# Optimization experiments

Hardware: AMD Instinct MI355X
Metric: run time of the kernel (lower is better)

## Reference

```python
import jax, jax.numpy as jnp
import numpy as np

B = 64        # batch
V1 = 4096     # nodes, layer 1 (D)
V2 = 1024     # nodes after pool/4
DF = 8        # input features (DFeat)
K1 = 25       # Chebyshev order layer 1
K2 = 25       # Chebyshev order layer 2
F1 = 32       # CL1_F
F2 = 64       # CL2_F
FC1F = 512    # FC1_F
FC2F = 10     # FC2_F
E1 = 65536    # nnz of L1
E2 = 16384    # nnz of L2
FC1Fin = F2 * (V1 // 16)  # 16384


def setup_inputs() -> dict:
    key = jax.random.key(0)
    ks = jax.random.split(key, 16)
    x = jax.random.normal(ks[0], (B, V1, DF), jnp.float32)
    L1_rows = jax.random.randint(ks[1], (E1,), 0, V1, dtype=jnp.int32)
    L1_cols = jax.random.randint(ks[2], (E1,), 0, V1, dtype=jnp.int32)
    # small values keep the order-25 Chebyshev recursion numerically tame
    L1_vals = jax.random.normal(ks[3], (E1,), jnp.float32) * 0.05
    L2_rows = jax.random.randint(ks[4], (E2,), 0, V2, dtype=jnp.int32)
    L2_cols = jax.random.randint(ks[5], (E2,), 0, V2, dtype=jnp.int32)
    L2_vals = jax.random.normal(ks[6], (E2,), jnp.float32) * 0.05

    def glorot(k, shape, fin, fout):
        s = np.sqrt(2.0 / (fin + fout)).astype(np.float32)
        return jax.random.uniform(k, shape, jnp.float32, -s, s)

    cl1_w = glorot(ks[7], (F1, K1 * DF), K1, F1)
    cl1_b = jnp.zeros((F1,), jnp.float32)
    cl2_w = glorot(ks[8], (F2, K2 * F1), K2 * F1, F2)
    cl2_b = jnp.zeros((F2,), jnp.float32)
    fc1_w = glorot(ks[9], (FC1F, FC1Fin), FC1Fin, FC1F)
    fc1_b = jnp.zeros((FC1F,), jnp.float32)
    fc2_w = glorot(ks[10], (FC2F, FC1F), FC1F, FC2F)
    fc2_b = jnp.zeros((FC2F,), jnp.float32)
    return dict(x=x, L1_rows=L1_rows, L1_cols=L1_cols, L1_vals=L1_vals,
                L2_rows=L2_rows, L2_cols=L2_cols, L2_vals=L2_vals,
                cl1_w=cl1_w, cl1_b=cl1_b, cl2_w=cl2_w, cl2_b=cl2_b,
                fc1_w=fc1_w, fc1_b=fc1_b, fc2_w=fc2_w, fc2_b=fc2_b)


def _cheb_conv(x, rows, cols, vals, W, b, K):
    """Chebyshev graph conv. x: [B, V, Fin]; sparse L as COO edge lists."""
    Bb, V, Fin = x.shape
    x0 = x.transpose(1, 2, 0).reshape(V, Fin * Bb)  # [V, Fin*B]

    def spmm(y):  # sparse [V,V] @ dense [V, C]
        return jax.ops.segment_sum(vals[:, None] * y[cols], rows, num_segments=V)

    x1 = spmm(x0)

    def step(carry, _):
        xm2, xm1 = carry
        xk = 2.0 * spmm(xm1) - xm2
        return (xm1, xk), xk

    _, rest = jax.lax.scan(step, (x0, x1), None, length=K - 2)
    stack = jnp.concatenate([x0[None], x1[None], rest], axis=0)  # [K, V, Fin*B]
    # [K,V,Fin,B] -> [B,V,Fin,K] -> [B*V, Fin*K], matching torch layout
    feat = stack.reshape(K, V, Fin, Bb).transpose(3, 1, 2, 0).reshape(Bb * V, Fin * K)
    out = feat @ W.T + b
    return out.reshape(Bb, V, -1)


def _max_pool(x, p):
    Bb, V, F = x.shape
    return x.reshape(Bb, V // p, p, F).max(axis=2)


def reference(x, L1_rows, L1_cols, L1_vals, L2_rows, L2_cols, L2_vals,
              cl1_w, cl1_b, cl2_w, cl2_b, fc1_w, fc1_b, fc2_w, fc2_b):
    h = _cheb_conv(x, L1_rows, L1_cols, L1_vals, cl1_w, cl1_b, K1)
    h = jax.nn.relu(h)
    h = _max_pool(h, 4)                                   # [B, V/4, F1]
    h = _cheb_conv(h, L2_rows, L2_cols, L2_vals, cl2_w, cl2_b, K2)
    h = jax.nn.relu(h)
    h = _max_pool(h, 4)                                   # [B, V/16, F2]
    h = h.reshape(-1, FC1Fin)
    h = jax.nn.relu(h @ fc1_w.T + fc1_b)
    # dropout treated as identity (eval mode / d=0)
    return h @ fc2_w.T + fc2_b                            # [B, FC2F]
```

## Files before the change

kernel.cpp:

```cpp
#include <hip/hip_runtime.h>
#include <hip/hip_fp16.h>

#define B_    64
#define V1_   4096
#define V2_   1024
#define DF_   8
#define K_    25
#define NP_   13
#define F1_   32
#define F2_   64
#define FC1F_ 512
#define FC2F_ 10
#define E1_   65536
#define E2_   16384
#define C1_   512
#define C2_   2048
#define FCIN_ 16384

typedef short bf16x8 __attribute__((ext_vector_type(8)));
typedef float f32x4  __attribute__((ext_vector_type(4)));

#define FMA_MIX_LO(acc, qv, gv) \
    asm("v_fma_mix_f32 %0, %1, %2, %0 op_sel:[1,0,0] op_sel_hi:[1,1,0]" \
        : "+v"(acc) : "v"(qv), "v"(gv))
#define FMA_MIX_HI(acc, qv, gv) \
    asm("v_fma_mix_f32 %0, %1, %2, %0 op_sel:[1,1,0] op_sel_hi:[1,1,0]" \
        : "+v"(acc) : "v"(qv), "v"(gv))

__device__ __forceinline__ unsigned short f2bf(float x) {
    unsigned u = __float_as_uint(x);
    u += 0x7FFFu + ((u >> 16) & 1u);
    return (unsigned short)(u >> 16);
}
__device__ __forceinline__ float h2f_lo(unsigned u) {
    return __half2float(__ushort_as_half((unsigned short)(u & 0xFFFFu)));
}
__device__ __forceinline__ float h2f_hi(unsigned u) {
    return __half2float(__ushort_as_half((unsigned short)(u >> 16)));
}

__global__ __launch_bounds__(256) void k_transpose_x(const float* __restrict__ x,
                                                     float* __restrict__ X0T) {
    __shared__ float tsh[DF_][B_][16];
    const int t = threadIdx.x;
    const int v0 = blockIdx.x * 16;
    for (int rep = 0; rep < 4; ++rep) {
        int idx = rep*256 + t;
        int b = idx >> 4, vv = idx & 15;
        const float4* p = (const float4*)&x[((size_t)b*V1_ + v0 + vv)*DF_];
        float4 a0 = p[0], a1 = p[1];
        tsh[0][b][vv]=a0.x; tsh[1][b][vv]=a0.y; tsh[2][b][vv]=a0.z; tsh[3][b][vv]=a0.w;
        tsh[4][b][vv]=a1.x; tsh[5][b][vv]=a1.y; tsh[6][b][vv]=a1.z; tsh[7][b][vv]=a1.w;
    }
    __syncthreads();
    for (int rep = 0; rep < 32; ++rep) {
        int idx = rep*256 + t;
        int vv = idx & 15, b = (idx >> 4) & 63, fin = idx >> 10;
        X0T[(size_t)(fin*64 + b)*V1_ + v0 + vv] = tsh[fin][b][vv];
    }
}

__global__ __launch_bounds__(256) void k_count(const int* __restrict__ rows, int E,
                                               int* __restrict__ cnt) {
    int e = blockIdx.x*256 + threadIdx.x;
    if (e < E) atomicAdd(&cnt[rows[e]], 1);
}

__global__ __launch_bounds__(256) void k_scan(const int* __restrict__ cnt, int V,
                                              int* __restrict__ offs, int* __restrict__ cursor) {
    __shared__ int psum[256];
    int t = threadIdx.x;
    int chunk = V >> 8;
    int lo = t*chunk;
    int s = 0;
    for (int i = lo; i < lo+chunk; ++i) s += (cnt[i] + 3) & ~3;
    psum[t] = s;
    __syncthreads();
    for (int off = 1; off < 256; off <<= 1) {
        int val = (t >= off) ? psum[t-off] : 0;
        __syncthreads();
        psum[t] += val;
        __syncthreads();
    }
    int run = (t == 0) ? 0 : psum[t-1];
    for (int i = lo; i < lo+chunk; ++i) {
        offs[i] = run; cursor[i] = run;
        run += (cnt[i] + 3) & ~3;
    }
    if (t == 255) offs[V] = run;
}

__global__ __launch_bounds__(256) void k_scatter(const int* __restrict__ rows,
                                                 const int* __restrict__ cols,
                                                 const float* __restrict__ vals, int E,
                                                 int shift,
                                                 int* __restrict__ cursor,
                                                 unsigned* __restrict__ ep) {
    int e = blockIdx.x*256 + threadIdx.x;
    if (e < E) {
        int p = atomicAdd(&cursor[rows[e]], 1);
        unsigned hv = (unsigned)__half_as_ushort(__float2half(vals[e]));
        ep[p] = (hv << 16) | ((unsigned)cols[e] << shift);
    }
}

template<int V, int THREADS, int MINW>
__global__ __launch_bounds__(THREADS, MINW) void k_cheb1(
        const float* __restrict__ X0T,
        const int* __restrict__ offs,
        const unsigned* __restrict__ ep,
        unsigned* __restrict__ stk) {
    constexpr int RPT = V / THREADS;
    __shared__ unsigned buf[2*V];
    const int c0 = blockIdx.x*2;
    const int t = threadIdx.x;
    int e0r[RPT], e1r[RPT];
    unsigned tlo0[RPT], tlo1[RPT];
    unsigned* __restrict__ p0 = stk + (size_t)(c0+0)*NP_*V;
    unsigned* __restrict__ p1 = stk + (size_t)(c0+1)*NP_*V;

#pragma unroll
    for (int r = 0; r < RPT; ++r) {
        const int v = r*THREADS + t;
        e0r[r] = offs[v]; e1r[r] = offs[v+1];
        const float x0 = X0T[(size_t)c0*V + v];
        const float x1 = X0T[(size_t)(c0+1)*V + v];
        __half2 hh = __floats2half2_rn(x0, x1);
        buf[v] = *(const unsigned*)&hh;
        tlo0[r] = f2bf(x0); tlo1[r] = f2bf(x1);
    }
    __syncthreads();

    auto step = [&](const unsigned* __restrict__ src, unsigned* __restrict__ dst,
                    bool first, bool last, int plane) {
#pragma unroll
        for (int r = 0; r < RPT; ++r) {
            const int v = r*THREADS + t;
            float s0a=0.f,s0b=0.f,s0c=0.f,s0d=0.f;
            float s1a=0.f,s1b=0.f,s1c=0.f,s1d=0.f;
            const int ee0 = e0r[r], ee1 = e1r[r];
            uint4 q = *(const uint4*)&ep[ee0];
            for (int e = ee0; e < ee1; e += 4) {
                const uint4 qn = *(const uint4*)&ep[e + 4];
                const unsigned g0 = *(const unsigned*)((const char*)src + (q.x & 0xFFFFu));
                const unsigned g1 = *(const unsigned*)((const char*)src + (q.y & 0xFFFFu));
                const unsigned g2 = *(const unsigned*)((const char*)src + (q.z & 0xFFFFu));
                const unsigned g3 = *(const unsigned*)((const char*)src + (q.w & 0xFFFFu));
                FMA_MIX_LO(s0a, q.x, g0); FMA_MIX_HI(s1a, q.x, g0);
                FMA_MIX_LO(s0b, q.y, g1); FMA_MIX_HI(s1b, q.y, g1);
                FMA_MIX_LO(s0c, q.z, g2); FMA_MIX_HI(s1c, q.z, g2);
                FMA_MIX_LO(s0d, q.w, g3); FMA_MIX_HI(s1d, q.w, g3);
                q = qn;
            }
            const float g0s = (s0a+s0b)+(s0c+s0d);
            const float g1s = (s1a+s1b)+(s1c+s1d);
            float xn0, xn1;
            if (first) { xn0 = g0s; xn1 = g1s; }
            else {
                const unsigned old = dst[v];
                xn0 = fmaf(2.f, g0s, -h2f_lo(old));
                xn1 = fmaf(2.f, g1s, -h2f_hi(old));
            }
            if (!last) {
                __half2 hh = __floats2half2_rn(xn0, xn1);
                dst[v] = *(const unsigned*)&hh;
            }
            const unsigned h0 = f2bf(xn0), h1 = f2bf(xn1);
            if (plane < 0) { tlo0[r] = h0; tlo1[r] = h1; }
            else {
                p0[(size_t)plane*V + v] = tlo0[r] | (h0 << 16);
                p1[(size_t)plane*V + v] = tlo1[r] | (h1 << 16);
            }
        }
        __syncthreads();
    };

    step(buf, buf + V, true, false, 0);
    for (int k = 2; k < 24; k += 2) {
        step(buf + V, buf, false, false, -1);
        step(buf, buf + V, false, false, (k + 1) >> 1);
    }
    step(buf + V, buf, false, true, -1);

#pragma unroll
    for (int r = 0; r < RPT; ++r) {
        const int v = r*THREADS + t;
        p0[(size_t)12*V + v] = tlo0[r];
        p1[(size_t)12*V + v] = tlo1[r];
    }
}

template<int V, int THREADS, int MINW>
__global__ __launch_bounds__(THREADS, MINW) void k_cheb2(
        const float* __restrict__ X0T,
        const int* __restrict__ offs,
        const unsigned* __restrict__ ep,
        unsigned* __restrict__ stk) {
    constexpr int RPT = V / THREADS;
    __shared__ uint2 buf[2*V];
    const int c0 = blockIdx.x*4;
    const int t = threadIdx.x;
    int e0r[RPT], e1r[RPT];
    unsigned tlo[RPT][4];
    unsigned* __restrict__ pl[4];
#pragma unroll
    for (int j = 0; j < 4; ++j) pl[j] = stk + (size_t)(c0+j)*NP_*V;

#pragma unroll
    for (int r = 0; r < RPT; ++r) {
        const int v = r*THREADS + t;
        e0r[r] = offs[v]; e1r[r] = offs[v+1];
        float xj[4];
#pragma unroll
        for (int j = 0; j < 4; ++j) {
            xj[j] = X0T[(size_t)(c0+j)*V + v];
            tlo[r][j] = f2bf(xj[j]);
        }
        __half2 ha = __floats2half2_rn(xj[0], xj[1]);
        __half2 hb = __floats2half2_rn(xj[2], xj[3]);
        buf[v] = make_uint2(*(const unsigned*)&ha, *(const unsigned*)&hb);
    }
    __syncthreads();

    auto step = [&](const uint2* __restrict__ src, uint2* __restrict__ dst,
                    bool first, bool last, int plane) {
#pragma unroll
        for (int r = 0; r < RPT; ++r) {
            const int v = r*THREADS + t;
            float acc[4][4];
#pragma unroll
            for (int j = 0; j < 4; ++j)
#pragma unroll
                for (int i = 0; i < 4; ++i) acc[j][i] = 0.f;
            const int ee0 = e0r[r], ee1 = e1r[r];
            uint4 q = *(const uint4*)&ep[ee0];
            for (int e = ee0; e < ee1; e += 4) {
                const uint4 qn = *(const uint4*)&ep[e + 4];
                const uint2 g0 = *(const uint2*)((const char*)src + (q.x & 0xFFFFu));
                const uint2 g1 = *(const uint2*)((const char*)src + (q.y & 0xFFFFu));
                const uint2 g2 = *(const uint2*)((const char*)src + (q.z & 0xFFFFu));
                const uint2 g3 = *(const uint2*)((const char*)src + (q.w & 0xFFFFu));
                FMA_MIX_LO(acc[0][0], q.x, g0.x); FMA_MIX_HI(acc[1][0], q.x, g0.x);
                FMA_MIX_LO(acc[2][0], q.x, g0.y); FMA_MIX_HI(acc[3][0], q.x, g0.y);
                FMA_MIX_LO(acc[0][1], q.y, g1.x); FMA_MIX_HI(acc[1][1], q.y, g1.x);
                FMA_MIX_LO(acc[2][1], q.y, g1.y); FMA_MIX_HI(acc[3][1], q.y, g1.y);
                FMA_MIX_LO(acc[0][2], q.z, g2.x); FMA_MIX_HI(acc[1][2], q.z, g2.x);
                FMA_MIX_LO(acc[2][2], q.z, g2.y); FMA_MIX_HI(acc[3][2], q.z, g2.y);
                FMA_MIX_LO(acc[0][3], q.w, g3.x); FMA_MIX_HI(acc[1][3], q.w, g3.x);
                FMA_MIX_LO(acc[2][3], q.w, g3.y); FMA_MIX_HI(acc[3][3], q.w, g3.y);
                q = qn;
            }
            float gs[4];
#pragma unroll
            for (int j = 0; j < 4; ++j)
                gs[j] = (acc[j][0]+acc[j][1])+(acc[j][2]+acc[j][3]);
            float xn[4];
            if (first) {
#pragma unroll
                for (int j = 0; j < 4; ++j) xn[j] = gs[j];
            } else {
                const uint2 old = dst[v];
                xn[0] = fmaf(2.f, gs[0], -h2f_lo(old.x));
                xn[1] = fmaf(2.f, gs[1], -h2f_hi(old.x));
                xn[2] = fmaf(2.f, gs[2], -h2f_lo(old.y));
                xn[3] = fmaf(2.f, gs[3], -h2f_hi(old.y));
            }
            if (!last) {
                __half2 ha = __floats2half2_rn(xn[0], xn[1]);
                __half2 hb = __floats2half2_rn(xn[2], xn[3]);
                dst[v] = make_uint2(*(const unsigned*)&ha, *(const unsigned*)&hb);
            }
            unsigned h[4];
#pragma unroll
            for (int j = 0; j < 4; ++j) h[j] = f2bf(xn[j]);
            if (plane < 0) {
#pragma unroll
                for (int j = 0; j < 4; ++j) tlo[r][j] = h[j];
            } else {
#pragma unroll
                for (int j = 0; j < 4; ++j)
                    pl[j][(size_t)plane*V + v] = tlo[r][j] | (h[j] << 16);
            }
        }
        __syncthreads();
    };

    step(buf, buf + V, true, false, 0);
    for (int k = 2; k < 24; k += 2) {
        step(buf + V, buf, false, false, -1);
        step(buf, buf + V, false, false, (k + 1) >> 1);
    }
    step(buf + V, buf, false, true, -1);

#pragma unroll
    for (int r = 0; r < RPT; ++r) {
        const int v = r*THREADS + t;
#pragma unroll
        for (int j = 0; j < 4; ++j)
            pl[j][(size_t)12*V + v] = tlo[r][j];
    }
}

template<int FIN, int F>
__global__ __launch_bounds__(256) void k_wprep(const float* __restrict__ W,
                                               unsigned short* __restrict__ Wb) {
    int idx = blockIdx.x*256 + threadIdx.x;
    int kk  = idx & 7;
    int f   = (idx >> 3) % F;
    int g   = (idx >> 3) / F % 4;
    int fin = idx / (8*F*4);
    int k = g*8 + kk;
    Wb[idx] = (k < K_) ? f2bf(W[(size_t)f*(FIN*K_) + fin*K_ + k]) : 0;
}

__global__ __launch_bounds__(256) void k_gemm1(const unsigned* __restrict__ STK,
                                               const unsigned short* __restrict__ Wb,
                                               const float* __restrict__ bias,
                                               float* __restrict__ X0T2) {
    __shared__ float Tsm[32][36];
    const int t = threadIdx.x, lane = t & 63, wave = t >> 6;
    const int b = blockIdx.x;
    const int v0 = blockIdx.y*128 + wave*32;
    const int m = lane & 15, g = lane >> 4;
    int offp[4];
#pragma unroll
    for (int p = 0; p < 4; ++p) {
        int pl = 4*g + p; if (pl > 12) pl = 12;
        offp[p] = pl*V1_ + v0 + m;
    }

    f32x4 acc[2][2];
#pragma unroll
    for (int mt = 0; mt < 2; ++mt)
#pragma unroll
        for (int ft = 0; ft < 2; ++ft) acc[mt][ft] = (f32x4){0.f,0.f,0.f,0.f};

#pragma unroll
    for (int fin = 0; fin < DF_; ++fin) {
        const unsigned* sp = STK + (size_t)(fin*64 + b)*(NP_*V1_);
        unsigned ua[4], ub[4];
#pragma unroll
        for (int p = 0; p < 4; ++p) { ua[p] = sp[offp[p]]; ub[p] = sp[offp[p] + 16]; }
        bf16x8 a0, a1;
        __builtin_memcpy(&a0, ua, 16);
        __builtin_memcpy(&a1, ub, 16);
        const bf16x8 w0 = *(const bf16x8*)&Wb[((fin*4+g)*F1_ + m)*8];
        const bf16x8 w1 = *(const bf16x8*)&Wb[((fin*4+g)*F1_ + 16 + m)*8];
        acc[0][0] = __builtin_amdgcn_mfma_f32_16x16x32_bf16(a0, w0, acc[0][0], 0,0,0);
        acc[0][1] = __builtin_amdgcn_mfma_f32_16x16x32_bf16(a0, w1, acc[0][1], 0,0,0);
        acc[1][0] = __builtin_amdgcn_mfma_f32_16x16x32_bf16(a1, w0, acc[1][0], 0,0,0);
        acc[1][1] = __builtin_amdgcn_mfma_f32_16x16x32_bf16(a1, w1, acc[1][1], 0,0,0);
    }
    float bv[2] = { bias[m], bias[16+m] };
#pragma unroll
    for (int mt = 0; mt < 2; ++mt)
#pragma unroll
        for (int ft = 0; ft < 2; ++ft) {
            f32x4 a = acc[mt][ft];
            float mx = fmaxf(fmaxf(a[0],a[1]), fmaxf(a[2],a[3])) + bv[ft];
            Tsm[ft*16 + m][wave*8 + mt*4 + g] = fmaxf(mx, 0.f);
        }
    __syncthreads();
    const int f = t >> 3, vg = t & 7;
    float4 o = *(const float4*)&Tsm[f][vg*4];
    *(float4*)&X0T2[(size_t)(f*64+b)*V2_ + blockIdx.y*32 + vg*4] = o;
}

__global__ __launch_bounds__(256) void k_gemm2(const unsigned* __restrict__ STK,
                                               const unsigned short* __restrict__ Wb,
                                               const float* __restrict__ bias,
                                               float* __restrict__ FCINT) {
    const int t = threadIdx.x, lane = t & 63, wave = t >> 6;
    const int b = blockIdx.x;
    const int v0 = blockIdx.y*128 + wave*32;
    const int m = lane & 15, g = lane >> 4;
    int offp[4];
#pragma unroll
    for (int p = 0; p < 4; ++p) {
        int pl = 4*g + p; if (pl > 12) pl = 12;
        offp[p] = pl*V2_ + v0 + m;
    }

    f32x4 acc[2][4];
#pragma unroll
    for (int mt = 0; mt < 2; ++mt)
#pragma unroll
        for (int ft = 0; ft < 4; ++ft) acc[mt][ft] = (f32x4){0.f,0.f,0.f,0.f};

#pragma unroll 4
    for (int fin = 0; fin < F1_; ++fin) {
        const unsigned* sp = STK + (size_t)(fin*64 + b)*(NP_*V2_);
        unsigned ua[4], ub[4];
#pragma unroll
        for (int p = 0; p < 4; ++p) { ua[p] = sp[offp[p]]; ub[p] = sp[offp[p] + 16]; }
        bf16x8 a0, a1;
        __builtin_memcpy(&a0, ua, 16);
        __builtin_memcpy(&a1, ub, 16);
#pragma unroll
        for (int ft = 0; ft < 4; ++ft) {
            const bf16x8 bw = *(const bf16x8*)&Wb[((fin*4+g)*F2_ + ft*16 + m)*8];
            acc[0][ft] = __builtin_amdgcn_mfma_f32_16x16x32_bf16(a0, bw, acc[0][ft], 0,0,0);
            acc[1][ft] = __builtin_amdgcn_mfma_f32_16x16x32_bf16(a1, bw, acc[1][ft], 0,0,0);
        }
    }
#pragma unroll
    for (int mt = 0; mt < 2; ++mt)
#pragma unroll
        for (int ft = 0; ft < 4; ++ft) {
            f32x4 a = acc[mt][ft];
            float mx = fmaxf(fmaxf(a[0],a[1]), fmaxf(a[2],a[3])) + bias[ft*16 + m];
            mx = fmaxf(mx, 0.f);
            int v2 = blockIdx.y*32 + wave*8 + mt*4 + g;
            FCINT[((size_t)v2*64 + ft*16 + m)*64 + b] = mx;
        }
}

__global__ __launch_bounds__(256) void k_fc1_init(const float* __restrict__ bias,
                                                  float* __restrict__ O) {
    int idx = blockIdx.x*256 + threadIdx.x;
    O[idx] = bias[idx & (FC1F_-1)];
}

__global__ __launch_bounds__(256) void k_fc1(const float* __restrict__ AT,
                                             const float* __restrict__ W,
                                             float* __restrict__ O) {
    const int t = threadIdx.x;
    const int b = t & 63;
    const int jq = __builtin_amdgcn_readfirstlane(t >> 6);
    const int j0 = blockIdx.x*32 + jq*8;
    const int i0 = blockIdx.y*1024;
    float acc[8] = {};
    for (int i = i0; i < i0 + 1024; i += 4) {
        float a0 = AT[(size_t)(i+0)*64 + b];
        float a1 = AT[(size_t)(i+1)*64 + b];
        float a2 = AT[(size_t)(i+2)*64 + b];
        float a3 = AT[(size_t)(i+3)*64 + b];
#pragma unroll
        for (int jj = 0; jj < 8; ++jj) {
            const float* wp = &W[(size_t)(j0+jj)*FCIN_ + i];
            acc[jj] = fmaf(a0, wp[0], acc[jj]);
            acc[jj] = fmaf(a1, wp[1], acc[jj]);
            acc[jj] = fmaf(a2, wp[2], acc[jj]);
            acc[jj] = fmaf(a3, wp[3], acc[jj]);
        }
    }
#pragma unroll
    for (int jj = 0; jj < 8; ++jj)
        atomicAdd(&O[b*FC1F_ + j0 + jj], acc[jj]);
}

__global__ void k_fc2(const float* __restrict__ O1, const float* __restrict__ W2,
                      const float* __restrict__ b2, float* __restrict__ out) {
    int c = blockIdx.x;
    int b = threadIdx.x;
    float s = b2[c];
    for (int j = 0; j < FC1F_; ++j)
        s = fmaf(fmaxf(O1[b*FC1F_ + j], 0.f), W2[c*FC1F_ + j], s);
    out[b*FC2F_ + c] = s;
}

extern "C" void kernel_launch(void* const* d_in, const int* in_sizes, int n_in,
                              void* d_out, int out_size, void* d_ws, size_t ws_size,
                              hipStream_t stream) {
    const float* x   = (const float*)d_in[0];
    const int*   l1r = (const int*)d_in[1];
    const int*   l1c = (const int*)d_in[2];
    const float* l1v = (const float*)d_in[3];
    const int*   l2r = (const int*)d_in[4];
    const int*   l2c = (const int*)d_in[5];
    const float* l2v = (const float*)d_in[6];
    const float* w1  = (const float*)d_in[7];
    const float* b1  = (const float*)d_in[8];
    const float* w2  = (const float*)d_in[9];
    const float* b2  = (const float*)d_in[10];
    const float* fw1 = (const float*)d_in[11];
    const float* fb1 = (const float*)d_in[12];
    const float* fw2 = (const float*)d_in[13];
    const float* fb2 = (const float*)d_in[14];
    float* out = (float*)d_out;

    char* wsp = (char*)d_ws;
    size_t off = 0;
    auto alloc = [&](size_t bytes) -> void* {
        void* p = wsp + off;
        off += (bytes + 255) & ~size_t(255);
        return p;
    };
    float*    X0T1  = (float*)alloc((size_t)C1_*V1_*4);
    unsigned* STACK = (unsigned*)alloc((size_t)C1_*NP_*V1_*4);
    float*    X0T2  = (float*)alloc((size_t)C2_*V2_*4);
    float*    FCINT = (float*)alloc((size_t)FCIN_*B_*4);
    float*    FC1O  = (float*)alloc((size_t)B_*FC1F_*4);
    unsigned short* WB1 = (unsigned short*)alloc((size_t)DF_*4*F1_*8*2);
    unsigned short* WB2 = (unsigned short*)alloc((size_t)F1_*4*F2_*8*2);
    int*      cnt1  = (int*)alloc(V1_*4);
    int*      offs1 = (int*)alloc((V1_+1)*4);
    int*      cur1  = (int*)alloc(V1_*4);
    unsigned* ep1   = (unsigned*)alloc((size_t)(E1_ + 4*V1_ + 8)*4);
    int*      cnt2  = (int*)alloc(V2_*4);
    int*      offs2 = (int*)alloc((V2_+1)*4);
    int*      cur2  = (int*)alloc(V2_*4);
    unsigned* ep2   = (unsigned*)alloc((size_t)(E2_ + 4*V2_ + 8)*4);

    hipMemsetAsync(cnt1, 0, V1_*4, stream);
    hipMemsetAsync(ep1, 0, (size_t)(E1_ + 4*V1_ + 8)*4, stream);
    hipMemsetAsync(cnt2, 0, V2_*4, stream);
    hipMemsetAsync(ep2, 0, (size_t)(E2_ + 4*V2_ + 8)*4, stream);
    hipLaunchKernelGGL(k_count,   dim3(E1_/256), dim3(256), 0, stream, l1r, E1_, cnt1);
    hipLaunchKernelGGL(k_scan,    dim3(1),       dim3(256), 0, stream, cnt1, V1_, offs1, cur1);
    hipLaunchKernelGGL(k_scatter, dim3(E1_/256), dim3(256), 0, stream, l1r, l1c, l1v, E1_, 2, cur1, ep1);
    hipLaunchKernelGGL(k_count,   dim3(E2_/256), dim3(256), 0, stream, l2r, E2_, cnt2);
    hipLaunchKernelGGL(k_scan,    dim3(1),       dim3(256), 0, stream, cnt2, V2_, offs2, cur2);
    hipLaunchKernelGGL(k_scatter, dim3(E2_/256), dim3(256), 0, stream, l2r, l2c, l2v, E2_, 3, cur2, ep2);
    hipLaunchKernelGGL((k_wprep<DF_,F1_>), dim3(DF_*4*F1_*8/256), dim3(256), 0, stream, w1, WB1);
    hipLaunchKernelGGL((k_wprep<F1_,F2_>), dim3(F1_*4*F2_*8/256), dim3(256), 0, stream, w2, WB2);

    hipLaunchKernelGGL(k_transpose_x, dim3(V1_/16), dim3(256), 0, stream, x, X0T1);
    hipLaunchKernelGGL((k_cheb1<V1_,1024,4>), dim3(C1_/2), dim3(1024), 0, stream,
                       X0T1, offs1, ep1, STACK);
    hipLaunchKernelGGL(k_gemm1, dim3(64, 32), dim3(256), 0, stream, STACK, WB1, b1, X0T2);

    hipLaunchKernelGGL((k_cheb2<V2_,512,4>), dim3(C2_/4), dim3(512), 0, stream,
                       X0T2, offs2, ep2, STACK);
    hipLaunchKernelGGL(k_gemm2, dim3(64, 8), dim3(256), 0, stream, STACK, WB2, b2, FCINT);

    hipLaunchKernelGGL(k_fc1_init, dim3(B_*FC1F_/256), dim3(256), 0, stream, fb1, FC1O);
    hipLaunchKernelGGL(k_fc1, dim3(16, 16), dim3(256), 0, stream, FCINT, fw1, FC1O);
    hipLaunchKernelGGL(k_fc2, dim3(FC2F_), dim3(B_), 0, stream, FC1O, fw2, fb2, out);
}
```

Before: 640.6 us.

## Split layer-1 Chebyshev rows across block pairs with global flag exchange

The layer-1 Chebyshev kernel now processes four channels per block, packed as two half2 values in shared memory, so each edge gather serves twice as many columns. Each channel group's node rows are split across two cooperating blocks. After every recursion step the two blocks trade their half of the new vector through a global exchange buffer, synchronised with release/acquire flag spin-waits. The intent is to keep the same 256-block grid with a 64KB shared buffer while halving per-block edge work. The risks are deadlock if the paired blocks are not co-resident, plus added per-step global traffic and spin latency.

```diff
diff --git a/kernel.cpp b/kernel.cpp
--- a/kernel.cpp
+++ b/kernel.cpp
@@ -16,6 +16,7 @@
 #define C1_   512
 #define C2_   2048
 #define FCIN_ 16384
+#define NPAIR1_ (C1_/4)
 
 typedef short bf16x8 __attribute__((ext_vector_type(8)));
 typedef float f32x4  __attribute__((ext_vector_type(4)));
@@ -104,89 +105,139 @@
     }
 }
 
-template<int V, int THREADS, int MINW>
-__global__ __launch_bounds__(THREADS, MINW) void k_cheb1(
+template<int V, int THREADS>
+__global__ __launch_bounds__(THREADS, 4) void k_cheb1(
         const float* __restrict__ X0T,
         const int* __restrict__ offs,
         const unsigned* __restrict__ ep,
-        unsigned* __restrict__ stk) {
-    constexpr int RPT = V / THREADS;
-    __shared__ unsigned buf[2*V];
-    const int c0 = blockIdx.x*2;
+        unsigned* __restrict__ stk,
+        uint2* __restrict__ xchg,
+        int* __restrict__ flags) {
+    constexpr int HV  = V/2;
+    constexpr int RPT = HV / THREADS;
+    __shared__ uint2 buf[2*V];
+    const int p = blockIdx.x >> 1, h = blockIdx.x & 1;
+    const int c0 = p*4;
+    const int row0 = h*HV;
     const int t = threadIdx.x;
     int e0r[RPT], e1r[RPT];
-    unsigned tlo0[RPT], tlo1[RPT];
-    unsigned* __restrict__ p0 = stk + (size_t)(c0+0)*NP_*V;
-    unsigned* __restrict__ p1 = stk + (size_t)(c0+1)*NP_*V;
-
+    unsigned tlo[RPT][4];
+    unsigned* __restrict__ pl[4];
+#pragma unroll
+    for (int j = 0; j < 4; ++j) pl[j] = stk + (size_t)(c0+j)*NP_*V;
+
+    for (int i = 0; i < V/THREADS; ++i) {
+        const int v = i*THREADS + t;
+        float xj[4];
+#pragma unroll
+        for (int j = 0; j < 4; ++j) xj[j] = X0T[(size_t)(c0+j)*V + v];
+        __half2 ha = __floats2half2_rn(xj[0], xj[1]);
+        __half2 hb = __floats2half2_rn(xj[2], xj[3]);
+        buf[v] = make_uint2(*(const unsigned*)&ha, *(const unsigned*)&hb);
+    }
 #pragma unroll
     for (int r = 0; r < RPT; ++r) {
-        const int v = r*THREADS + t;
+        const int v = row0 + r*THREADS + t;
         e0r[r] = offs[v]; e1r[r] = offs[v+1];
-        const float x0 = X0T[(size_t)c0*V + v];
-        const float x1 = X0T[(size_t)(c0+1)*V + v];
-        __half2 hh = __floats2half2_rn(x0, x1);
-        buf[v] = *(const unsigned*)&hh;
-        tlo0[r] = f2bf(x0); tlo1[r] = f2bf(x1);
+#pragma unroll
+        for (int j = 0; j < 4; ++j) tlo[r][j] = f2bf(X0T[(size_t)(c0+j)*V + v]);
     }
     __syncthreads();
 
-    auto step = [&](const unsigned* __restrict__ src, unsigned* __restrict__ dst,
-                    bool first, bool last, int plane) {
+    for (int k = 1; k <= 24; ++k) {
+        const bool first = (k == 1), last = (k == 24);
+        const int plane = (k & 1) ? (k >> 1) : -1;
+        const uint2* __restrict__ src = buf + ((k & 1) ? 0 : V);
+        uint2*       __restrict__ dst = buf + ((k & 1) ? V : 0);
+        const int xbase = (((k & 1)*NPAIR1_ + p)*2 + h)*HV;
+
 #pragma unroll
         for (int r = 0; r < RPT; ++r) {
-            const int v = r*THREADS + t;
-            float s0a=0.f,s0b=0.f,s0c=0.f,s0d=0.f;
-            float s1a=0.f,s1b=0.f,s1c=0.f,s1d=0.f;
+            const int v = row0 + r*THREADS + t;
+            float acc[4][4];
+#pragma unroll
+            for (int j = 0; j < 4; ++j)
+#pragma unroll
+                for (int i = 0; i < 4; ++i) acc[j][i] = 0.f;
             const int ee0 = e0r[r], ee1 = e1r[r];
             uint4 q = *(const uint4*)&ep[ee0];
             for (int e = ee0; e < ee1; e += 4) {
                 const uint4 qn = *(const uint4*)&ep[e + 4];
-                const unsigned g0 = *(const unsigned*)((const char*)src + (q.x & 0xFFFFu));
-                const unsigned g1 = *(const unsigned*)((const char*)src + (q.y & 0xFFFFu));
-                const unsigned g2 = *(const unsigned*)((const char*)src + (q.z & 0xFFFFu));
-                const unsigned g3 = *(const unsigned*)((const char*)src + (q.w & 0xFFFFu));
-                FMA_MIX_LO(s0a, q.x, g0); FMA_MIX_HI(s1a, q.x, g0);
-                FMA_MIX_LO(s0b, q.y, g1); FMA_MIX_HI(s1b, q.y, g1);
-                FMA_MIX_LO(s0c, q.z, g2); FMA_MIX_HI(s1c, q.z, g2);
-                FMA_MIX_LO(s0d, q.w, g3); FMA_MIX_HI(s1d, q.w, g3);
+                const uint2 g0 = *(const uint2*)((const char*)src + (q.x & 0xFFFFu));
+                const uint2 g1 = *(const uint2*)((const char*)src + (q.y & 0xFFFFu));
+                const uint2 g2 = *(const uint2*)((const char*)src + (q.z & 0xFFFFu));
+                const uint2 g3 = *(const uint2*)((const char*)src + (q.w & 0xFFFFu));
+                FMA_MIX_LO(acc[0][0], q.x, g0.x); FMA_MIX_HI(acc[1][0], q.x, g0.x);
+                FMA_MIX_LO(acc[2][0], q.x, g0.y); FMA_MIX_HI(acc[3][0], q.x, g0.y);
+                FMA_MIX_LO(acc[0][1], q.y, g1.x); FMA_MIX_HI(acc[1][1], q.y, g1.x);
+                FMA_MIX_LO(acc[2][1], q.y, g1.y); FMA_MIX_HI(acc[3][1], q.y, g1.y);
+                FMA_MIX_LO(acc[0][2], q.z, g2.x); FMA_MIX_HI(acc[1][2], q.z, g2.x);
+                FMA_MIX_LO(acc[2][2], q.z, g2.y); FMA_MIX_HI(acc[3][2], q.z, g2.y);
+                FMA_MIX_LO(acc[0][3], q.w, g3.x); FMA_MIX_HI(acc[1][3], q.w, g3.x);
+                FMA_MIX_LO(acc[2][3], q.w, g3.y); FMA_MIX_HI(acc[3][3], q.w, g3.y);
                 q = qn;
             }
-            const float g0s = (s0a+s0b)+(s0c+s0d);
-            const float g1s = (s1a+s1b)+(s1c+s1d);
-            float xn0, xn1;
-            if (first) { xn0 = g0s; xn1 = g1s; }
-            else {
-                const unsigned old = dst[v];
-                xn0 = fmaf(2.f, g0s, -h2f_lo(old));
-                xn1 = fmaf(2.f, g1s, -h2f_hi(old));
-            }
+            float gs[4], xn[4];
+#pragma unroll
+            for (int j = 0; j < 4; ++j)
+                gs[j] = (acc[j][0]+acc[j][1])+(acc[j][2]+acc[j][3]);
+            if (first) {
+#pragma unroll
+                for (int j = 0; j < 4; ++j) xn[j] = gs[j];
+            } else {
+                const uint2 old = dst[v];
+                xn[0] = fmaf(2.f, gs[0], -h2f_lo(old.x));
+                xn[1] = fmaf(2.f, gs[1], -h2f_hi(old.x));
+                xn[2] = fmaf(2.f, gs[2], -h2f_lo(old.y));
+                xn[3] = fmaf(2.f, gs[3], -h2f_hi(old.y));
+            }
+            __half2 ha = __floats2half2_rn(xn[0], xn[1]);
+            __half2 hb = __floats2half2_rn(xn[2], xn[3]);
+            const uint2 pk = make_uint2(*(const unsigned*)&ha, *(const unsigned*)&hb);
             if (!last) {
-                __half2 hh = __floats2half2_rn(xn0, xn1);
-                dst[v] = *(const unsigned*)&hh;
-            }
-            const unsigned h0 = f2bf(xn0), h1 = f2bf(xn1);
-            if (plane < 0) { tlo0[r] = h0; tlo1[r] = h1; }
-            else {
-                p0[(size_t)plane*V + v] = tlo0[r] | (h0 << 16);
-                p1[(size_t)plane*V + v] = tlo1[r] | (h1 << 16);
+                dst[v] = pk;
+                xchg[xbase + (v - row0)] = pk;
+            }
+            unsigned hh[4];
+#pragma unroll
+            for (int j = 0; j < 4; ++j) hh[j] = f2bf(xn[j]);
+            if (plane < 0) {
+#pragma unroll
+                for (int j = 0; j < 4; ++j) tlo[r][j] = hh[j];
+            } else {
+#pragma unroll
+                for (int j = 0; j < 4; ++j)
+                    pl[j][(size_t)plane*V + v] = tlo[r][j] | (hh[j] << 16);
+            }
+        }
+        if (!last) {
+            __syncthreads();
+            if (t == 0) {
+                __threadfence();
+                __hip_atomic_store(&flags[p*2 + h], k, __ATOMIC_RELEASE,
+                                   __HIP_MEMORY_SCOPE_AGENT);
+                while (__hip_atomic_load(&flags[p*2 + (1-h)], __ATOMIC_ACQUIRE,
+                                         __HIP_MEMORY_SCOPE_AGENT) < k) {}
+                __threadfence();
+            }
+            __syncthreads();
+            const int pbase = (((k & 1)*NPAIR1_ + p)*2 + (1-h))*HV;
+            const int prow0 = (1-h)*HV;
+#pragma unroll
+            for (int r = 0; r < RPT; ++r) {
+                const int vv = r*THREADS + t;
+                dst[prow0 + vv] = xchg[pbase + vv];
             }
         }
         __syncthreads();
-    };
-
-    step(buf, buf + V, true, false, 0);
-    for (int k = 2; k < 24; k += 2) {
-        step(buf + V, buf, false, false, -1);
-        step(buf, buf + V, false, false, (k + 1) >> 1);
-    }
-    step(buf + V, buf, false, true, -1);
+    }
 
 #pragma unroll
     for (int r = 0; r < RPT; ++r) {
-        const int v = r*THREADS + t;
-        p0[(size_t)12*V + v] = tlo0[r];
-        p1[(size_t)12*V + v] = tlo1[r];
+        const int v = row0 + r*THREADS + t;
+#pragma unroll
+        for (int j = 0; j < 4; ++j)
+            pl[j][(size_t)12*V + v] = tlo[r][j];
     }
 }
 
@@ -493,6 +544,8 @@
     float*    FC1O  = (float*)alloc((size_t)B_*FC1F_*4);
     unsigned short* WB1 = (unsigned short*)alloc((size_t)DF_*4*F1_*8*2);
     unsigned short* WB2 = (unsigned short*)alloc((size_t)F1_*4*F2_*8*2);
+    uint2*    XCHG  = (uint2*)alloc((size_t)2*NPAIR1_*2*(V1_/2)*8);
+    int*      FLAGS = (int*)alloc((size_t)NPAIR1_*2*4);
     int*      cnt1  = (int*)alloc(V1_*4);
     int*      offs1 = (int*)alloc((V1_+1)*4);
     int*      cur1  = (int*)alloc(V1_*4);
@@ -506,9 +559,10 @@
     hipMemsetAsync(ep1, 0, (size_t)(E1_ + 4*V1_ + 8)*4, stream);
     hipMemsetAsync(cnt2, 0, V2_*4, stream);
     hipMemsetAsync(ep2, 0, (size_t)(E2_ + 4*V2_ + 8)*4, stream);
+    hipMemsetAsync(FLAGS, 0, (size_t)NPAIR1_*2*4, stream);
     hipLaunchKernelGGL(k_count,   dim3(E1_/256), dim3(256), 0, stream, l1r, E1_, cnt1);
     hipLaunchKernelGGL(k_scan,    dim3(1),       dim3(256), 0, stream, cnt1, V1_, offs1, cur1);
-    hipLaunchKernelGGL(k_scatter, dim3(E1_/256), dim3(256), 0, stream, l1r, l1c, l1v, E1_, 2, cur1, ep1);
+    hipLaunchKernelGGL(k_scatter, dim3(E1_/256), dim3(256), 0, stream, l1r, l1c, l1v, E1_, 3, cur1, ep1);
     hipLaunchKernelGGL(k_count,   dim3(E2_/256), dim3(256), 0, stream, l2r, E2_, cnt2);
     hipLaunchKernelGGL(k_scan,    dim3(1),       dim3(256), 0, stream, cnt2, V2_, offs2, cur2);
     hipLaunchKernelGGL(k_scatter, dim3(E2_/256), dim3(256), 0, stream, l2r, l2c, l2v, E2_, 3, cur2, ep2);
@@ -516,8 +570,8 @@
     hipLaunchKernelGGL((k_wprep<F1_,F2_>), dim3(F1_*4*F2_*8/256), dim3(256), 0, stream, w2, WB2);
 
     hipLaunchKernelGGL(k_transpose_x, dim3(V1_/16), dim3(256), 0, stream, x, X0T1);
-    hipLaunchKernelGGL((k_cheb1<V1_,1024,4>), dim3(C1_/2), dim3(1024), 0, stream,
-                       X0T1, offs1, ep1, STACK);
+    hipLaunchKernelGGL((k_cheb1<V1_,1024>), dim3(NPAIR1_*2), dim3(1024), 0, stream,
+                       X0T1, offs1, ep1, STACK, XCHG, FLAGS);
     hipLaunchKernelGGL(k_gemm1, dim3(64, 32), dim3(256), 0, stream, STACK, WB1, b1, X0T2);
 
     hipLaunchKernelGGL((k_cheb2<V2_,512,4>), dim3(C2_/4), dim3(512), 0, stream,
```

New measurement: 1.068 ms. 66.7% more time.

## Restructure layer-1 Chebyshev as per-order row-major SpMM launches with fused pooled GEMM

Applied to the files above, without the earlier changes.

Replaces the block-per-channel-pair layer-1 Chebyshev kernel, which kept the whole recursion in LDS, with 24 separate kernel launches. Each launch does one SpMM over a node-major fp16 layout where a wave gathers full 1 KB rows per neighbour. The bf16 stack is now stored node-major per order, and a new GEMM kernel reads it, applies the weights with MFMA, and does bias, ReLU and 4-way max-pool in registers. The intent is coalesced wide gathers and better parallelism. The cost is 24 launches, global-memory round trips between orders, and strided 2-byte A-operand loads in the GEMM.

```diff
diff --git a/kernel.cpp b/kernel.cpp
--- a/kernel.cpp
+++ b/kernel.cpp
@@ -39,8 +39,9 @@
     return __half2float(__ushort_as_half((unsigned short)(u >> 16)));
 }
 
-__global__ __launch_bounds__(256) void k_transpose_x(const float* __restrict__ x,
-                                                     float* __restrict__ X0T) {
+__global__ __launch_bounds__(256) void k_transpose_rm(const float* __restrict__ x,
+                                                      unsigned* __restrict__ XP,
+                                                      unsigned* __restrict__ stk0) {
     __shared__ float tsh[DF_][B_][16];
     const int t = threadIdx.x;
     const int v0 = blockIdx.x * 16;
@@ -53,10 +54,14 @@
         tsh[4][b][vv]=a1.x; tsh[5][b][vv]=a1.y; tsh[6][b][vv]=a1.z; tsh[7][b][vv]=a1.w;
     }
     __syncthreads();
-    for (int rep = 0; rep < 32; ++rep) {
+    for (int rep = 0; rep < 16; ++rep) {
         int idx = rep*256 + t;
-        int vv = idx & 15, b = (idx >> 4) & 63, fin = idx >> 10;
-        X0T[(size_t)(fin*64 + b)*V1_ + v0 + vv] = tsh[fin][b][vv];
+        int c2 = idx & 255, vv = idx >> 8;
+        int c = c2*2, fin = c >> 6, b = c & 63;
+        float xa = tsh[fin][b][vv], xb = tsh[fin][b+1][vv];
+        __half2 hh = __floats2half2_rn(xa, xb);
+        XP[(size_t)(v0+vv)*256 + c2]   = *(const unsigned*)&hh;
+        stk0[(size_t)(v0+vv)*256 + c2] = (unsigned)f2bf(xa) | ((unsigned)f2bf(xb) << 16);
     }
 }
 
@@ -104,90 +109,153 @@
     }
 }
 
-template<int V, int THREADS, int MINW>
-__global__ __launch_bounds__(THREADS, MINW) void k_cheb1(
-        const float* __restrict__ X0T,
+__global__ __launch_bounds__(512) void k_dcheb1(int k,
+        const unsigned short* __restrict__ Xsrc,
+        unsigned short* __restrict__ Xown,
+        unsigned short* __restrict__ stk16,
         const int* __restrict__ offs,
-        const unsigned* __restrict__ ep,
-        unsigned* __restrict__ stk) {
-    constexpr int RPT = V / THREADS;
-    __shared__ unsigned buf[2*V];
-    const int c0 = blockIdx.x*2;
+        const unsigned* __restrict__ ep) {
     const int t = threadIdx.x;
-    int e0r[RPT], e1r[RPT];
-    unsigned tlo0[RPT], tlo1[RPT];
-    unsigned* __restrict__ p0 = stk + (size_t)(c0+0)*NP_*V;
-    unsigned* __restrict__ p1 = stk + (size_t)(c0+1)*NP_*V;
-
-#pragma unroll
-    for (int r = 0; r < RPT; ++r) {
-        const int v = r*THREADS + t;
-        e0r[r] = offs[v]; e1r[r] = offs[v+1];
-        const float x0 = X0T[(size_t)c0*V + v];
-        const float x1 = X0T[(size_t)(c0+1)*V + v];
-        __half2 hh = __floats2half2_rn(x0, x1);
-        buf[v] = *(const unsigned*)&hh;
-        tlo0[r] = f2bf(x0); tlo1[r] = f2bf(x1);
-    }
-    __syncthreads();
-
-    auto step = [&](const unsigned* __restrict__ src, unsigned* __restrict__ dst,
-                    bool first, bool last, int plane) {
-#pragma unroll
-        for (int r = 0; r < RPT; ++r) {
-            const int v = r*THREADS + t;
-            float s0a=0.f,s0b=0.f,s0c=0.f,s0d=0.f;
-            float s1a=0.f,s1b=0.f,s1c=0.f,s1d=0.f;
-            const int ee0 = e0r[r], ee1 = e1r[r];
-            uint4 q = *(const uint4*)&ep[ee0];
-            for (int e = ee0; e < ee1; e += 4) {
-                const uint4 qn = *(const uint4*)&ep[e + 4];
-                const unsigned g0 = *(const unsigned*)((const char*)src + (q.x & 0xFFFFu));
-                const unsigned g1 = *(const unsigned*)((const char*)src + (q.y & 0xFFFFu));
-                const unsigned g2 = *(const unsigned*)((const char*)src + (q.z & 0xFFFFu));
-                const unsigned g3 = *(const unsigned*)((const char*)src + (q.w & 0xFFFFu));
-                FMA_MIX_LO(s0a, q.x, g0); FMA_MIX_HI(s1a, q.x, g0);
-                FMA_MIX_LO(s0b, q.y, g1); FMA_MIX_HI(s1b, q.y, g1);
-                FMA_MIX_LO(s0c, q.z, g2); FMA_MIX_HI(s1c, q.z, g2);
-                FMA_MIX_LO(s0d, q.w, g3); FMA_MIX_HI(s1d, q.w, g3);
-                q = qn;
-            }
-            const float g0s = (s0a+s0b)+(s0c+s0d);
-            const float g1s = (s1a+s1b)+(s1c+s1d);
-            float xn0, xn1;
-            if (first) { xn0 = g0s; xn1 = g1s; }
-            else {
-                const unsigned old = dst[v];
-                xn0 = fmaf(2.f, g0s, -h2f_lo(old));
-                xn1 = fmaf(2.f, g1s, -h2f_hi(old));
-            }
-            if (!last) {
-                __half2 hh = __floats2half2_rn(xn0, xn1);
-                dst[v] = *(const unsigned*)&hh;
-            }
-            const unsigned h0 = f2bf(xn0), h1 = f2bf(xn1);
-            if (plane < 0) { tlo0[r] = h0; tlo1[r] = h1; }
-            else {
-                p0[(size_t)plane*V + v] = tlo0[r] | (h0 << 16);
-                p1[(size_t)plane*V + v] = tlo1[r] | (h1 << 16);
+    const int lane = t & 63;
+    const int v = blockIdx.x*8 + (t >> 6);
+    const int e0 = offs[v], e1 = offs[v+1];
+    const unsigned loff = (unsigned)lane * 16u;
+    float acc[8];
+#pragma unroll
+    for (int j = 0; j < 8; ++j) acc[j] = 0.f;
+    const char* srcb = (const char*)Xsrc;
+
+    for (int e = e0; e < e1; e += 4) {
+        const uint4 q = *(const uint4*)&ep[e];
+        const uint4 g0 = *(const uint4*)(srcb + ((q.x & 0xFFFFu)*1024u + loff));
+        const uint4 g1 = *(const uint4*)(srcb + ((q.y & 0xFFFFu)*1024u + loff));
+        const uint4 g2 = *(const uint4*)(srcb + ((q.z & 0xFFFFu)*1024u + loff));
+        const uint4 g3 = *(const uint4*)(srcb + ((q.w & 0xFFFFu)*1024u + loff));
+        FMA_MIX_LO(acc[0], q.x, g0.x); FMA_MIX_HI(acc[1], q.x, g0.x);
+        FMA_MIX_LO(acc[2], q.x, g0.y); FMA_MIX_HI(acc[3], q.x, g0.y);
+        FMA_MIX_LO(acc[4], q.x, g0.z); FMA_MIX_HI(acc[5], q.x, g0.z);
+        FMA_MIX_LO(acc[6], q.x, g0.w); FMA_MIX_HI(acc[7], q.x, g0.w);
+        FMA_MIX_LO(acc[0], q.y, g1.x); FMA_MIX_HI(acc[1], q.y, g1.x);
+        FMA_MIX_LO(acc[2], q.y, g1.y); FMA_MIX_HI(acc[3], q.y, g1.y);
+        FMA_MIX_LO(acc[4], q.y, g1.z); FMA_MIX_HI(acc[5], q.y, g1.z);
+        FMA_MIX_LO(acc[6], q.y, g1.w); FMA_MIX_HI(acc[7], q.y, g1.w);
+        FMA_MIX_LO(acc[0], q.z, g2.x); FMA_MIX_HI(acc[1], q.z, g2.x);
+        FMA_MIX_LO(acc[2], q.z, g2.y); FMA_MIX_HI(acc[3], q.z, g2.y);
+        FMA_MIX_LO(acc[4], q.z, g2.z); FMA_MIX_HI(acc[5], q.z, g2.z);
+        FMA_MIX_LO(acc[6], q.z, g2.w); FMA_MIX_HI(acc[7], q.z, g2.w);
+        FMA_MIX_LO(acc[0], q.w, g3.x); FMA_MIX_HI(acc[1], q.w, g3.x);
+        FMA_MIX_LO(acc[2], q.w, g3.y); FMA_MIX_HI(acc[3], q.w, g3.y);
+        FMA_MIX_LO(acc[4], q.w, g3.z); FMA_MIX_HI(acc[5], q.w, g3.z);
+        FMA_MIX_LO(acc[6], q.w, g3.w); FMA_MIX_HI(acc[7], q.w, g3.w);
+    }
+
+    float xn[8];
+    if (k > 1) {
+        const uint4 old = *(const uint4*)((const char*)Xown + ((size_t)v*1024 + loff));
+        xn[0] = fmaf(2.f, acc[0], -h2f_lo(old.x));
+        xn[1] = fmaf(2.f, acc[1], -h2f_hi(old.x));
+        xn[2] = fmaf(2.f, acc[2], -h2f_lo(old.y));
+        xn[3] = fmaf(2.f, acc[3], -h2f_hi(old.y));
+        xn[4] = fmaf(2.f, acc[4], -h2f_lo(old.z));
+        xn[5] = fmaf(2.f, acc[5], -h2f_hi(old.z));
+        xn[6] = fmaf(2.f, acc[6], -h2f_lo(old.w));
+        xn[7] = fmaf(2.f, acc[7], -h2f_hi(old.w));
+    } else {
+#pragma unroll
+        for (int j = 0; j < 8; ++j) xn[j] = acc[j];
+    }
+
+    uint4 hp;
+    { __half2 h0 = __floats2half2_rn(xn[0], xn[1]); hp.x = *(const unsigned*)&h0;
+      __half2 h1 = __floats2half2_rn(xn[2], xn[3]); hp.y = *(const unsigned*)&h1;
+      __half2 h2 = __floats2half2_rn(xn[4], xn[5]); hp.z = *(const unsigned*)&h2;
+      __half2 h3 = __floats2half2_rn(xn[6], xn[7]); hp.w = *(const unsigned*)&h3; }
+    *(uint4*)((char*)Xown + ((size_t)v*1024 + loff)) = hp;
+
+    uint4 bp;
+    bp.x = (unsigned)f2bf(xn[0]) | ((unsigned)f2bf(xn[1]) << 16);
+    bp.y = (unsigned)f2bf(xn[2]) | ((unsigned)f2bf(xn[3]) << 16);
+    bp.z = (unsigned)f2bf(xn[4]) | ((unsigned)f2bf(xn[5]) << 16);
+    bp.w = (unsigned)f2bf(xn[6]) | ((unsigned)f2bf(xn[7]) << 16);
+    *(uint4*)((char*)stk16 + (((size_t)k*V1_ + v)*1024 + loff)) = bp;
+}
+
+template<int FIN, int F>
+__global__ __launch_bounds__(256) void k_wprep(const float* __restrict__ W,
+                                               unsigned short* __restrict__ Wb) {
+    int idx = blockIdx.x*256 + threadIdx.x;
+    int kk  = idx & 7;
+    int f   = (idx >> 3) % F;
+    int g   = (idx >> 3) / F % 4;
+    int fin = idx / (8*F*4);
+    int k = g*8 + kk;
+    Wb[idx] = (k < K_) ? f2bf(W[(size_t)f*(FIN*K_) + fin*K_ + k]) : 0;
+}
+
+__global__ __launch_bounds__(256) void k_gemm1b(const unsigned short* __restrict__ stk16,
+                                                const unsigned short* __restrict__ Wb,
+                                                const float* __restrict__ bias,
+                                                float* __restrict__ X0T2) {
+    const int t = threadIdx.x, lane = t & 63, wave = t >> 6;
+    const int v2 = blockIdx.x*4 + wave;
+    const int m = lane & 15, g = lane >> 4;
+    int kbase[8];
+#pragma unroll
+    for (int j = 0; j < 8; ++j) {
+        int kq = g*8 + j; if (kq > 24) kq = 24;
+        kbase[j] = kq * (V1_*C1_);
+    }
+    float bv[2] = { bias[m], bias[16+m] };
+    f32x4 pool[4][2];
+
+    for (int vv = 0; vv < 4; ++vv) {
+        const int v = v2*4 + vv;
+        f32x4 acc[4][2];
+#pragma unroll
+        for (int mt = 0; mt < 4; ++mt)
+#pragma unroll
+            for (int ft = 0; ft < 2; ++ft) acc[mt][ft] = (f32x4){0.f,0.f,0.f,0.f};
+
+        for (int fin = 0; fin < DF_; ++fin) {
+            const int cbase = v*C1_ + fin*64 + m;
+            const bf16x8 bw0 = *(const bf16x8*)&Wb[((fin*4+g)*F1_ + m)*8];
+            const bf16x8 bw1 = *(const bf16x8*)&Wb[((fin*4+g)*F1_ + 16 + m)*8];
+#pragma unroll
+            for (int mt = 0; mt < 4; ++mt) {
+                unsigned short au[8];
+#pragma unroll
+                for (int j = 0; j < 8; ++j)
+                    au[j] = stk16[(size_t)(kbase[j] + cbase + mt*16)];
+                bf16x8 a;
+                __builtin_memcpy(&a, au, 16);
+                acc[mt][0] = __builtin_amdgcn_mfma_f32_16x16x32_bf16(a, bw0, acc[mt][0], 0,0,0);
+                acc[mt][1] = __builtin_amdgcn_mfma_f32_16x16x32_bf16(a, bw1, acc[mt][1], 0,0,0);
             }
         }
-        __syncthreads();
-    };
-
-    step(buf, buf + V, true, false, 0);
-    for (int k = 2; k < 24; k += 2) {
-        step(buf + V, buf, false, false, -1);
-        step(buf, buf + V, false, false, (k + 1) >> 1);
-    }
-    step(buf + V, buf, false, true, -1);
-
-#pragma unroll
-    for (int r = 0; r < RPT; ++r) {
-        const int v = r*THREADS + t;
-        p0[(size_t)12*V + v] = tlo0[r];
-        p1[(size_t)12*V + v] = tlo1[r];
-    }
+#pragma unroll
+        for (int mt = 0; mt < 4; ++mt)
+#pragma unroll
+            for (int ft = 0; ft < 2; ++ft) {
+                if (vv == 0) pool[mt][ft] = acc[mt][ft];
+                else {
+#pragma unroll
+                    for (int j = 0; j < 4; ++j)
+                        pool[mt][ft][j] = fmaxf(pool[mt][ft][j], acc[mt][ft][j]);
+                }
+            }
+    }
+
+#pragma unroll
+    for (int mt = 0; mt < 4; ++mt)
+#pragma unroll
+        for (int ft = 0; ft < 2; ++ft)
+#pragma unroll
+            for (int j = 0; j < 4; ++j) {
+                float mx = fmaxf(pool[mt][ft][j] + bv[ft], 0.f);
+                int b = mt*16 + g*4 + j;
+                int f = ft*16 + m;
+                X0T2[(size_t)(f*64+b)*V2_ + v2] = mx;
+            }
 }
 
 template<int V, int THREADS, int MINW>
@@ -299,71 +367,6 @@
         for (int j = 0; j < 4; ++j)
             pl[j][(size_t)12*V + v] = tlo[r][j];
     }
-}
-
-template<int FIN, int F>
-__global__ __launch_bounds__(256) void k_wprep(const float* __restrict__ W,
-                                               unsigned short* __restrict__ Wb) {
-    int idx = blockIdx.x*256 + threadIdx.x;
-    int kk  = idx & 7;
-    int f   = (idx >> 3) % F;
-    int g   = (idx >> 3) / F % 4;
-    int fin = idx / (8*F*4);
-    int k = g*8 + kk;
-    Wb[idx] = (k < K_) ? f2bf(W[(size_t)f*(FIN*K_) + fin*K_ + k]) : 0;
-}
-
-__global__ __launch_bounds__(256) void k_gemm1(const unsigned* __restrict__ STK,
-                                               const unsigned short* __restrict__ Wb,
-                                               const float* __restrict__ bias,
-                                               float* __restrict__ X0T2) {
-    __shared__ float Tsm[32][36];
-    const int t = threadIdx.x, lane = t & 63, wave = t >> 6;
-    const int b = blockIdx.x;
-    const int v0 = blockIdx.y*128 + wave*32;
-    const int m = lane & 15, g = lane >> 4;
-    int offp[4];
-#pragma unroll
-    for (int p = 0; p < 4; ++p) {
-        int pl = 4*g + p; if (pl > 12) pl = 12;
-        offp[p] = pl*V1_ + v0 + m;
-    }
-
-    f32x4 acc[2][2];
-#pragma unroll
-    for (int mt = 0; mt < 2; ++mt)
-#pragma unroll
-        for (int ft = 0; ft < 2; ++ft) acc[mt][ft] = (f32x4){0.f,0.f,0.f,0.f};
-
-#pragma unroll
-    for (int fin = 0; fin < DF_; ++fin) {
-        const unsigned* sp = STK + (size_t)(fin*64 + b)*(NP_*V1_);
-        unsigned ua[4], ub[4];
-#pragma unroll
-        for (int p = 0; p < 4; ++p) { ua[p] = sp[offp[p]]; ub[p] = sp[offp[p] + 16]; }
-        bf16x8 a0, a1;
-        __builtin_memcpy(&a0, ua, 16);
-        __builtin_memcpy(&a1, ub, 16);
-        const bf16x8 w0 = *(const bf16x8*)&Wb[((fin*4+g)*F1_ + m)*8];
-        const bf16x8 w1 = *(const bf16x8*)&Wb[((fin*4+g)*F1_ + 16 + m)*8];
-        acc[0][0] = __builtin_amdgcn_mfma_f32_16x16x32_bf16(a0, w0, acc[0][0], 0,0,0);
-        acc[0][1] = __builtin_amdgcn_mfma_f32_16x16x32_bf16(a0, w1, acc[0][1], 0,0,0);
-        acc[1][0] = __builtin_amdgcn_mfma_f32_16x16x32_bf16(a1, w0, acc[1][0], 0,0,0);
-        acc[1][1] = __builtin_amdgcn_mfma_f32_16x16x32_bf16(a1, w1, acc[1][1], 0,0,0);
-    }
-    float bv[2] = { bias[m], bias[16+m] };
-#pragma unroll
-    for (int mt = 0; mt < 2; ++mt)
-#pragma unroll
-        for (int ft = 0; ft < 2; ++ft) {
-            f32x4 a = acc[mt][ft];
-            float mx = fmaxf(fmaxf(a[0],a[1]), fmaxf(a[2],a[3])) + bv[ft];
-            Tsm[ft*16 + m][wave*8 + mt*4 + g] = fmaxf(mx, 0.f);
-        }
-    __syncthreads();
-    const int f = t >> 3, vg = t & 7;
-    float4 o = *(const float4*)&Tsm[f][vg*4];
-    *(float4*)&X0T2[(size_t)(f*64+b)*V2_ + blockIdx.y*32 + vg*4] = o;
 }
 
 __global__ __launch_bounds__(256) void k_gemm2(const unsigned* __restrict__ STK,
@@ -486,8 +489,11 @@
         off += (bytes + 255) & ~size_t(255);
         return p;
     };
-    float*    X0T1  = (float*)alloc((size_t)C1_*V1_*4);
-    unsigned* STACK = (unsigned*)alloc((size_t)C1_*NP_*V1_*4);
+    void*     STKU  = alloc((size_t)C2_*NP_*V2_*4);
+    unsigned short* stk16 = (unsigned short*)STKU;
+    unsigned*       STACK = (unsigned*)STKU;
+    unsigned short* XB0   = (unsigned short*)alloc((size_t)V1_*C1_*2);
+    unsigned short* XB1   = (unsigned short*)alloc((size_t)V1_*C1_*2);
     float*    X0T2  = (float*)alloc((size_t)C2_*V2_*4);
     float*    FCINT = (float*)alloc((size_t)FCIN_*B_*4);
     float*    FC1O  = (float*)alloc((size_t)B_*FC1F_*4);
@@ -508,17 +514,22 @@
     hipMemsetAsync(ep2, 0, (size_t)(E2_ + 4*V2_ + 8)*4, stream);
     hipLaunchKernelGGL(k_count,   dim3(E1_/256), dim3(256), 0, stream, l1r, E1_, cnt1);
     hipLaunchKernelGGL(k_scan,    dim3(1),       dim3(256), 0, stream, cnt1, V1_, offs1, cur1);
-    hipLaunchKernelGGL(k_scatter, dim3(E1_/256), dim3(256), 0, stream, l1r, l1c, l1v, E1_, 2, cur1, ep1);
+    hipLaunchKernelGGL(k_scatter, dim3(E1_/256), dim3(256), 0, stream, l1r, l1c, l1v, E1_, 0, cur1, ep1);
     hipLaunchKernelGGL(k_count,   dim3(E2_/256), dim3(256), 0, stream, l2r, E2_, cnt2);
     hipLaunchKernelGGL(k_scan,    dim3(1),       dim3(256), 0, stream, cnt2, V2_, offs2, cur2);
     hipLaunchKernelGGL(k_scatter, dim3(E2_/256), dim3(256), 0, stream, l2r, l2c, l2v, E2_, 3, cur2, ep2);
     hipLaunchKernelGGL((k_wprep<DF_,F1_>), dim3(DF_*4*F1_*8/256), dim3(256), 0, stream, w1, WB1);
     hipLaunchKernelGGL((k_wprep<F1_,F2_>), dim3(F1_*4*F2_*8/256), dim3(256), 0, stream, w2, WB2);
 
-    hipLaunchKernelGGL(k_transpose_x, dim3(V1_/16), dim3(256), 0, stream, x, X0T1);
-    hipLaunchKernelGGL((k_cheb1<V1_,1024,4>), dim3(C1_/2), dim3(1024), 0, stream,
-                       X0T1, offs1, ep1, STACK);
-    hipLaunchKernelGGL(k_gemm1, dim3(64, 32), dim3(256), 0, stream, STACK, WB1, b1, X0T2);
+    hipLaunchKernelGGL(k_transpose_rm, dim3(V1_/16), dim3(256), 0, stream,
+                       x, (unsigned*)XB0, (unsigned*)stk16);
+    for (int k = 1; k <= 24; ++k) {
+        unsigned short* src = (k & 1) ? XB0 : XB1;
+        unsigned short* own = (k & 1) ? XB1 : XB0;
+        hipLaunchKernelGGL(k_dcheb1, dim3(V1_/8), dim3(512), 0, stream,
+                           k, src, own, stk16, offs1, ep1);
+    }
+    hipLaunchKernelGGL(k_gemm1b, dim3(V2_/4), dim3(256), 0, stream, stk16, WB1, b1, X0T2);
 
     hipLaunchKernelGGL((k_cheb2<V2_,512,4>), dim3(C2_/4), dim3(512), 0, stream,
                        X0T2, offs2, ep2, STACK);
```

After: 630.1 us. About the same (-1.6%).
